# Kernel optimization log

Hardware: AMD Instinct MI355X
Metric: run time of the kernel (lower is better)

## Reference

```python
import jax, jax.numpy as jnp
import numpy as np

N = 50000          # nodes
E_RAW = 600000     # edges before self loops
FEAT = 64
HID = 64
HEADS = 4
NUM_SUBST = 32
NUM_GRAPHS = 128


def setup_inputs() -> dict:
    key = jax.random.key(0)
    ks = jax.random.split(key, 24)
    s = 0.05
    x = jax.random.normal(ks[0], (N, FEAT), jnp.float32)
    sids = jax.random.randint(ks[1], (N,), 0, NUM_SUBST)
    x = x.at[:, 5].set(sids.astype(jnp.float32))  # x[:,5] holds integer substructure ids
    edge_index = jax.random.randint(ks[2], (2, E_RAW), 0, N, dtype=jnp.int32)
    batch = jnp.sort(jax.random.randint(ks[3], (N,), 0, NUM_GRAPHS, dtype=jnp.int32))
    p = lambda i, shape: jax.random.normal(ks[i], shape, jnp.float32) * s
    return dict(
        x=x, edge_index=edge_index, batch=batch,
        # substructure attention MLP: Linear(FEAT,32) -> LeakyReLU(0.2) -> Linear(32,1)
        w_sa1=p(4, (FEAT, 32)), b_sa1=p(5, (32,)),
        w_sa2=p(6, (32, 1)), b_sa2=p(7, (1,)),
        # GATConv 1: in=FEAT+1, out=HID, heads=HEADS, concat
        W1=p(8, (FEAT + 1, HEADS * HID)), att_s1=p(9, (HEADS, HID)),
        att_d1=p(10, (HEADS, HID)), b1=p(11, (HEADS * HID,)),
        # GATConv 2: in=HEADS*HID, out=HID, heads=1
        W2=p(12, (HEADS * HID, HID)), att_s2=p(13, (1, HID)),
        att_d2=p(14, (1, HID)), b2=p(15, (HID,)),
        # prediction head
        Wp1=p(16, (HID, HID // 2)), bp1=p(17, (HID // 2,)),
        Wp2=p(18, (HID // 2, 1)), bp2=p(19, (1,)),
    )


def _gat_layer(h_in, src, dst, W, att_s, att_d, bias, n):
    heads, out_dim = att_s.shape
    h = (h_in @ W).reshape(n, heads, out_dim)            # [N, H, D]
    a_s = jnp.einsum('nhd,hd->nh', h, att_s)             # [N, H]
    a_d = jnp.einsum('nhd,hd->nh', h, att_d)
    e = jax.nn.leaky_relu(a_s[src] + a_d[dst], negative_slope=0.2)  # [E, H]
    m = jax.ops.segment_max(e, dst, num_segments=n)
    ex = jnp.exp(e - m[dst])
    denom = jax.ops.segment_sum(ex, dst, num_segments=n)
    alpha = ex / (denom[dst] + 1e-16)                    # segment softmax per dst node
    out = jax.ops.segment_sum(h[src] * alpha[..., None], dst, num_segments=n)
    return out.reshape(n, heads * out_dim) + bias        # concat heads + bias


def reference(x, edge_index, batch, w_sa1, b_sa1, w_sa2, b_sa2,
              W1, att_s1, att_d1, b1, W2, att_s2, att_d2, b2,
              Wp1, bp1, Wp2, bp2):
    n = x.shape[0]
    sid = jax.lax.stop_gradient(x[:, 5]).astype(jnp.int32)
    # segment mean of node features per substructure id (all NUM_SUBST ids present)
    cnt = jax.ops.segment_sum(jnp.ones((n,), x.dtype), sid, num_segments=NUM_SUBST)
    smean = jax.ops.segment_sum(x, sid, num_segments=NUM_SUBST) / jnp.maximum(cnt, 1.0)[:, None]
    logits = jax.nn.leaky_relu(smean @ w_sa1 + b_sa1, negative_slope=0.2) @ w_sa2 + b_sa2
    w = jax.nn.softmax(logits, axis=0)                   # [S, 1]
    atom_w = w[sid]                                      # broadcast back to atoms [N, 1]
    h = jnp.concatenate([x, atom_w], axis=1)             # [N, FEAT+1]
    # add_self_loops (gat2's remove+add self loops yields the same edge set)
    loops = jnp.arange(n, dtype=edge_index.dtype)
    src = jnp.concatenate([edge_index[0], loops])
    dst = jnp.concatenate([edge_index[1], loops])
    h = jax.nn.elu(_gat_layer(h, src, dst, W1, att_s1, att_d1, b1, n))
    h = _gat_layer(h, src, dst, W2, att_s2, att_d2, b2, n)
    g = jax.ops.segment_sum(h, batch, num_segments=NUM_GRAPHS)   # global_add_pool
    return jax.nn.elu(g @ Wp1 + bp1) @ Wp2 + bp2         # [NUM_GRAPHS, 1]
```

## Files before the change

### kernel.cpp

```cpp
#include <hip/hip_runtime.h>
#include <math.h>

#define N_NODES 50000
#define E_RAWN  600000
#define FEAT    64
#define HID     64
#define HEADS   4
#define NSUB    32
#define NGRAPH  128
#define NB_SCAN ((N_NODES + 255) / 256)
#define G2_NODES 128

__device__ __forceinline__ float leaky02(float v) { return v >= 0.f ? v : 0.2f * v; }
__device__ __forceinline__ float elu1(float v)    { return v > 0.f ? v : expm1f(v); }

__device__ __forceinline__ unsigned bf2pack(float a, float b) {
    unsigned ua = __float_as_uint(a), ub = __float_as_uint(b);
    ua = (ua + 0x7FFFu + ((ua >> 16) & 1u)) >> 16;
    ub = (ub + 0x7FFFu + ((ub >> 16) & 1u)) >> 16;
    return ua | (ub << 16);
}
__device__ __forceinline__ float bflo(unsigned p) { return __uint_as_float(p << 16); }
__device__ __forceinline__ float bfhi(unsigned p) { return __uint_as_float(p & 0xFFFF0000u); }
__device__ __forceinline__ float bfs(unsigned short v) { return __uint_as_float((unsigned)v << 16); }

__global__ void k_subst_accum(const float* __restrict__ x,
                              float* __restrict__ ssum, float* __restrict__ scnt) {
    __shared__ float lsum[NSUB * FEAT];
    __shared__ float lcnt[NSUB];
    int tid = threadIdx.x;
    for (int i = tid; i < NSUB * FEAT; i += blockDim.x) lsum[i] = 0.f;
    if (tid < NSUB) lcnt[tid] = 0.f;
    __syncthreads();
    const int total = N_NODES * FEAT;
    for (int idx = blockIdx.x * blockDim.x + tid; idx < total; idx += gridDim.x * blockDim.x) {
        int node = idx >> 6, f = idx & 63;
        int sid = (int)x[node * FEAT + 5];
        atomicAdd(&lsum[sid * FEAT + f], x[idx]);
        if (f == 0) atomicAdd(&lcnt[sid], 1.f);
    }
    __syncthreads();
    for (int i = tid; i < NSUB * FEAT; i += blockDim.x) atomicAdd(&ssum[i], lsum[i]);
    if (tid < NSUB) atomicAdd(&scnt[tid], lcnt[tid]);
}

__global__ void k_subst_mlp(const float* __restrict__ ssum, const float* __restrict__ scnt,
                            const float* __restrict__ w_sa1, const float* __restrict__ b_sa1,
                            const float* __restrict__ w_sa2, const float* __restrict__ b_sa2,
                            float* __restrict__ wsub) {
    __shared__ float logits[NSUB];
    int s = threadIdx.x;
    float cnt = fmaxf(scnt[s], 1.f);
    float sm[FEAT];
    for (int k = 0; k < FEAT; k++) sm[k] = ssum[s * FEAT + k] / cnt;
    float logit = b_sa2[0];
    for (int j = 0; j < 32; j++) {
        float hj = b_sa1[j];
        for (int k = 0; k < FEAT; k++) hj += sm[k] * w_sa1[k * 32 + j];
        hj = leaky02(hj);
        logit += hj * w_sa2[j];
    }
    logits[s] = logit;
    __syncthreads();
    float m = -1e30f;
    for (int i = 0; i < NSUB; i++) m = fmaxf(m, logits[i]);
    float dsum = 0.f;
    for (int i = 0; i < NSUB; i++) dsum += expf(logits[i] - m);
    wsub[s] = expf(logits[s] - m) / dsum;
}

__global__ __launch_bounds__(256) void k_gemm1(const float* __restrict__ x,
                                               const float* __restrict__ wsub,
                                               const float* __restrict__ W1,
                                               const float* __restrict__ att_s1,
                                               const float* __restrict__ att_d1,
                                               unsigned* __restrict__ h1b,
                                               float* __restrict__ as1, float* __restrict__ ad1) {
    __shared__ float xs[65][36];
    __shared__ float ws[16][260];
    int t = threadIdx.x;
    int gbase = blockIdx.x * 32;
    for (int idx = t; idx < 32 * 64; idx += 256) {
        int n = idx >> 6, f = idx & 63;
        int g = gbase + n;
        xs[f][n] = (g < N_NODES) ? x[(size_t)g * FEAT + f] : 0.f;
    }
    __syncthreads();
    if (t < 32) {
        int sid = (int)xs[5][t];
        xs[64][t] = wsub[sid & (NSUB - 1)];
    }

    int m = t & 31, q = t >> 5;
    int c0 = m * 8, n0 = q * 4;
    float accs[32];
    #pragma unroll
    for (int i = 0; i < 32; ++i) accs[i] = 0.f;

    for (int kc = 0; kc < 4; ++kc) {
        __syncthreads();
        #pragma unroll
        for (int s = 0; s < 16; ++s)
            ws[s][t] = W1[(size_t)(kc * 16 + s) * 256 + t];
        __syncthreads();
        #pragma unroll
        for (int kk = 0; kk < 16; ++kk) {
            float4 wa = *(const float4*)(&ws[kk][c0]);
            float4 wb = *(const float4*)(&ws[kk][c0 + 4]);
            float4 xv = *(const float4*)(&xs[kc * 16 + kk][n0]);
            float wv[8] = {wa.x, wa.y, wa.z, wa.w, wb.x, wb.y, wb.z, wb.w};
            float xj[4] = {xv.x, xv.y, xv.z, xv.w};
            #pragma unroll
            for (int c = 0; c < 8; ++c)
                #pragma unroll
                for (int j = 0; j < 4; ++j)
                    accs[c * 4 + j] += wv[c] * xj[j];
        }
    }
    {
        float4 wa = *(const float4*)(W1 + (size_t)64 * 256 + c0);
        float4 wb = *(const float4*)(W1 + (size_t)64 * 256 + c0 + 4);
        float4 xv = *(const float4*)(&xs[64][n0]);
        float wv[8] = {wa.x, wa.y, wa.z, wa.w, wb.x, wb.y, wb.z, wb.w};
        float xj[4] = {xv.x, xv.y, xv.z, xv.w};
        #pragma unroll
        for (int c = 0; c < 8; ++c)
            #pragma unroll
            for (int j = 0; j < 4; ++j)
                accs[c * 4 + j] += wv[c] * xj[j];
    }

    float atts[8], attd[8];
    #pragma unroll
    for (int c = 0; c < 8; ++c) { atts[c] = att_s1[c0 + c]; attd[c] = att_d1[c0 + c]; }
    int h = m >> 3;
    #pragma unroll
    for (int j = 0; j < 4; ++j) {
        int node = gbase + n0 + j;
        float ps = 0.f, pd = 0.f;
        #pragma unroll
        for (int c = 0; c < 8; ++c) { ps += accs[c * 4 + j] * atts[c]; pd += accs[c * 4 + j] * attd[c]; }
        ps += __shfl_xor(ps, 1, 64); pd += __shfl_xor(pd, 1, 64);
        ps += __shfl_xor(ps, 2, 64); pd += __shfl_xor(pd, 2, 64);
        ps += __shfl_xor(ps, 4, 64); pd += __shfl_xor(pd, 4, 64);
        if (node < N_NODES) {
            uint4 pk;
            pk.x = bf2pack(accs[0 * 4 + j], accs[1 * 4 + j]);
            pk.y = bf2pack(accs[2 * 4 + j], accs[3 * 4 + j]);
            pk.z = bf2pack(accs[4 * 4 + j], accs[5 * 4 + j]);
            pk.w = bf2pack(accs[6 * 4 + j], accs[7 * 4 + j]);
            *(uint4*)(h1b + (size_t)node * 128 + m * 4) = pk;
            if ((m & 7) == 0) { as1[node * 4 + h] = ps; ad1[node * 4 + h] = pd; }
        }
    }
}

__global__ void k_count(const int* __restrict__ dst, int* __restrict__ cnt) {
    int e = blockIdx.x * blockDim.x + threadIdx.x;
    if (e < E_RAWN) atomicAdd(&cnt[dst[e]], 1);
}

__global__ void k_scan1(const int* __restrict__ cnt, int* __restrict__ offs, int* __restrict__ bsum) {
    __shared__ int sd[256];
    int tid = threadIdx.x;
    int i = blockIdx.x * 256 + tid;
    int v = (i < N_NODES) ? cnt[i] : 0;
    sd[tid] = v;
    for (int off = 1; off < 256; off <<= 1) {
        __syncthreads();
        int tv = (tid >= off) ? sd[tid - off] : 0;
        __syncthreads();
        sd[tid] += tv;
    }
    __syncthreads();
    if (i < N_NODES) offs[i] = sd[tid] - v;
    if (tid == 255) bsum[blockIdx.x] = sd[255];
}

__global__ void k_scan2(int* __restrict__ bsum, int nb) {
    __shared__ int sd[256];
    int tid = threadIdx.x;
    int v = (tid < nb) ? bsum[tid] : 0;
    sd[tid] = v;
    for (int off = 1; off < 256; off <<= 1) {
        __syncthreads();
        int tv = (tid >= off) ? sd[tid - off] : 0;
        __syncthreads();
        sd[tid] += tv;
    }
    __syncthreads();
    if (tid < nb) bsum[tid] = sd[tid] - v;
}

__global__ void k_scan3(int* __restrict__ offs, const int* __restrict__ bsum) {
    int i = blockIdx.x * 256 + threadIdx.x;
    if (i < N_NODES) offs[i] += bsum[blockIdx.x];
    if (blockIdx.x == 0 && threadIdx.x == 0) offs[N_NODES] = E_RAWN;
}

__global__ void k_scatter(const int* __restrict__ src, const int* __restrict__ dst,
                          const int* __restrict__ offs, int* __restrict__ cur,
                          int* __restrict__ esrc) {
    int e = blockIdx.x * blockDim.x + threadIdx.x;
    if (e < E_RAWN) {
        int d = dst[e];
        int pos = offs[d] + atomicAdd(&cur[d], 1);
        esrc[pos] = src[e];
    }
}

__global__ __launch_bounds__(256) void k_gat1(const unsigned* __restrict__ h1b,
                                              const float* __restrict__ as1,
                                              const float* __restrict__ ad1,
                                              const int* __restrict__ offs,
                                              const int* __restrict__ esrc,
                                              const float* __restrict__ b1,
                                              unsigned* __restrict__ hactb) {
    int wave = threadIdx.x >> 6, lane = threadIdx.x & 63;
    int i = blockIdx.x * 4 + wave;
    if (i >= N_NODES) return;
    int beg = offs[i], end = offs[i + 1];
    int h = lane >> 4;
    float adv = ad1[i * 4 + h];
    float w0 = __expf(leaky02(as1[i * 4 + h] + adv));
    uint2 hv = *(const uint2*)(h1b + (size_t)i * 128 + lane * 2);
    float4 acc = make_float4(w0 * bflo(hv.x), w0 * bfhi(hv.x), w0 * bflo(hv.y), w0 * bfhi(hv.y));
    float d = w0;
    int p = beg;
    for (; p + 3 < end; p += 4) {
        int s0 = esrc[p], s1 = esrc[p + 1], s2 = esrc[p + 2], s3 = esrc[p + 3];
        uint2 hA = *(const uint2*)(h1b + (size_t)s0 * 128 + lane * 2);
        uint2 hB = *(const uint2*)(h1b + (size_t)s1 * 128 + lane * 2);
        uint2 hC = *(const uint2*)(h1b + (size_t)s2 * 128 + lane * 2);
        uint2 hD = *(const uint2*)(h1b + (size_t)s3 * 128 + lane * 2);
        float a0 = as1[s0 * 4 + h], a1 = as1[s1 * 4 + h];
        float a2 = as1[s2 * 4 + h], a3 = as1[s3 * 4 + h];
        float wA = __expf(leaky02(a0 + adv));
        float wB = __expf(leaky02(a1 + adv));
        float wC = __expf(leaky02(a2 + adv));
        float wD = __expf(leaky02(a3 + adv));
        d += (wA + wB) + (wC + wD);
        acc.x += wA * bflo(hA.x) + wB * bflo(hB.x) + wC * bflo(hC.x) + wD * bflo(hD.x);
        acc.y += wA * bfhi(hA.x) + wB * bfhi(hB.x) + wC * bfhi(hC.x) + wD * bfhi(hD.x);
        acc.z += wA * bflo(hA.y) + wB * bflo(hB.y) + wC * bflo(hC.y) + wD * bflo(hD.y);
        acc.w += wA * bfhi(hA.y) + wB * bfhi(hB.y) + wC * bfhi(hC.y) + wD * bfhi(hD.y);
    }
    for (; p < end; ++p) {
        int s0 = esrc[p];
        uint2 hA = *(const uint2*)(h1b + (size_t)s0 * 128 + lane * 2);
        float wA = __expf(leaky02(as1[s0 * 4 + h] + adv));
        d += wA;
        acc.x += wA * bflo(hA.x);
        acc.y += wA * bfhi(hA.x);
        acc.z += wA * bflo(hA.y);
        acc.w += wA * bfhi(hA.y);
    }
    float inv = 1.f / (d + 1e-16f);
    float4 bb = *(const float4*)(b1 + lane * 4);
    float rx = elu1(acc.x * inv + bb.x);
    float ry = elu1(acc.y * inv + bb.y);
    float rz = elu1(acc.z * inv + bb.z);
    float rw = elu1(acc.w * inv + bb.w);
    uint2 pk;
    pk.x = bf2pack(rx, ry);
    pk.y = bf2pack(rz, rw);
    *(uint2*)(hactb + (size_t)i * 128 + lane * 2) = pk;
}

__global__ __launch_bounds__(256) void k_gemm2(const unsigned* __restrict__ hactb,
                                               const float* __restrict__ W2,
                                               const float* __restrict__ att_s2,
                                               const float* __restrict__ att_d2,
                                               unsigned short* __restrict__ h2b,
                                               float* __restrict__ as2, float* __restrict__ ad2) {
    __shared__ float hs[G2_NODES][68];
    int t = threadIdx.x;
    int gbase = blockIdx.x * G2_NODES;
    int m = t & 7, q = t >> 3;
    int c0 = m * 8, n0 = q * 4;
    float accs[32];
    #pragma unroll
    for (int i = 0; i < 32; ++i) accs[i] = 0.f;

    int sn = t >> 3;
    int sko = t & 7;

    for (int kc = 0; kc < 4; ++kc) {
        __syncthreads();
        #pragma unroll
        for (int r = 0; r < 4; ++r) {
            int n = sn + r * 32;
            int g = gbase + n;
            uint4 v = (g < N_NODES)
                ? *(const uint4*)(hactb + (size_t)g * 128 + kc * 32 + sko * 4)
                : make_uint4(0u, 0u, 0u, 0u);
            float4 lo = make_float4(bflo(v.x), bfhi(v.x), bflo(v.y), bfhi(v.y));
            float4 hi = make_float4(bflo(v.z), bfhi(v.z), bflo(v.w), bfhi(v.w));
            *(float4*)(&hs[n][sko * 8])     = lo;
            *(float4*)(&hs[n][sko * 8 + 4]) = hi;
        }
        __syncthreads();
        const float* Wc = W2 + (size_t)kc * 64 * 64;
        for (int kk = 0; kk < 16; ++kk) {
            float4 xv0 = *(const float4*)(&hs[n0 + 0][kk * 4]);
            float4 xv1 = *(const float4*)(&hs[n0 + 1][kk * 4]);
            float4 xv2 = *(const float4*)(&hs[n0 + 2][kk * 4]);
            float4 xv3 = *(const float4*)(&hs[n0 + 3][kk * 4]);
            const float* x0 = (const float*)&xv0;
            const float* x1 = (const float*)&xv1;
            const float* x2 = (const float*)&xv2;
            const float* x3 = (const float*)&xv3;
            #pragma unroll
            for (int jj = 0; jj < 4; ++jj) {
                int k = kk * 4 + jj;
                float4 wa = *(const float4*)(Wc + (size_t)k * 64 + c0);
                float4 wb = *(const float4*)(Wc + (size_t)k * 64 + c0 + 4);
                float wv[8] = {wa.x, wa.y, wa.z, wa.w, wb.x, wb.y, wb.z, wb.w};
                float xj[4] = {x0[jj], x1[jj], x2[jj], x3[jj]};
                #pragma unroll
                for (int c = 0; c < 8; ++c)
                    #pragma unroll
                    for (int j = 0; j < 4; ++j)
                        accs[c * 4 + j] += wv[c] * xj[j];
            }
        }
    }

    float atts[8], attd[8];
    #pragma unroll
    for (int c = 0; c < 8; ++c) { atts[c] = att_s2[c0 + c]; attd[c] = att_d2[c0 + c]; }
    #pragma unroll
    for (int j = 0; j < 4; ++j) {
        int node = gbase + n0 + j;
        float ps = 0.f, pd = 0.f;
        #pragma unroll
        for (int c = 0; c < 8; ++c) { ps += accs[c * 4 + j] * atts[c]; pd += accs[c * 4 + j] * attd[c]; }
        ps += __shfl_xor(ps, 1, 64); pd += __shfl_xor(pd, 1, 64);
        ps += __shfl_xor(ps, 2, 64); pd += __shfl_xor(pd, 2, 64);
        ps += __shfl_xor(ps, 4, 64); pd += __shfl_xor(pd, 4, 64);
        if (node < N_NODES) {
            uint4 pk;
            pk.x = bf2pack(accs[0 * 4 + j], accs[1 * 4 + j]);
            pk.y = bf2pack(accs[2 * 4 + j], accs[3 * 4 + j]);
            pk.z = bf2pack(accs[4 * 4 + j], accs[5 * 4 + j]);
            pk.w = bf2pack(accs[6 * 4 + j], accs[7 * 4 + j]);
            *(uint4*)(h2b + (size_t)node * 64 + c0) = pk;
            if (m == 0) { as2[node] = ps; ad2[node] = pd; }
        }
    }
}

__global__ __launch_bounds__(256) void k_gat2(const unsigned short* __restrict__ h2b,
                                              const float* __restrict__ as2,
                                              const float* __restrict__ ad2,
                                              const int* __restrict__ offs,
                                              const int* __restrict__ esrc,
                                              float* __restrict__ rbuf) {
    int wave = threadIdx.x >> 6, lane = threadIdx.x & 63;
    int i = blockIdx.x * 4 + wave;
    if (i >= N_NODES) return;
    int beg = offs[i], end = offs[i + 1];
    float adv = ad2[i];
    float w0 = __expf(leaky02(as2[i] + adv));
    float d = w0;
    float acc = w0 * bfs(h2b[(size_t)i * 64 + lane]);
    int p = beg;
    for (; p + 3 < end; p += 4) {
        int s0 = esrc[p], s1 = esrc[p + 1], s2 = esrc[p + 2], s3 = esrc[p + 3];
        float hA = bfs(h2b[(size_t)s0 * 64 + lane]);
        float hB = bfs(h2b[(size_t)s1 * 64 + lane]);
        float hC = bfs(h2b[(size_t)s2 * 64 + lane]);
        float hD = bfs(h2b[(size_t)s3 * 64 + lane]);
        float wA = __expf(leaky02(as2[s0] + adv));
        float wB = __expf(leaky02(as2[s1] + adv));
        float wC = __expf(leaky02(as2[s2] + adv));
        float wD = __expf(leaky02(as2[s3] + adv));
        d += (wA + wB) + (wC + wD);
        acc += wA * hA + wB * hB + wC * hC + wD * hD;
    }
    for (; p < end; ++p) {
        int s0 = esrc[p];
        float wA = __expf(leaky02(as2[s0] + adv));
        d += wA;
        acc += wA * bfs(h2b[(size_t)s0 * 64 + lane]);
    }
    rbuf[(size_t)i * 64 + lane] = acc / (d + 1e-16f);
}

__device__ __forceinline__ int lower_bound_i(const int* a, int n, int v) {
    int lo = 0, hi = n;
    while (lo < hi) { int mid = (lo + hi) >> 1; if (a[mid] < v) lo = mid + 1; else hi = mid; }
    return lo;
}

__global__ void k_pool_head(const float* __restrict__ rbuf, const int* __restrict__ batch,
                            const float* __restrict__ b2,
                            const float* __restrict__ Wp1, const float* __restrict__ bp1,
                            const float* __restrict__ Wp2, const float* __restrict__ bp2,
                            float* __restrict__ out) {
    __shared__ float red[4][64];
    __shared__ float tot[64];
    __shared__ float hred[32];
    int b = blockIdx.x;
    int lo = lower_bound_i(batch, N_NODES, b);
    int hi = lower_bound_i(batch, N_NODES, b + 1);
    int t = threadIdx.x;
    int c = t & 63, rg = t >> 6;
    float s = 0.f;
    for (int r = lo + rg; r < hi; r += 4) s += rbuf[(size_t)r * 64 + c];
    red[rg][c] = s;
    __syncthreads();
    if (rg == 0) tot[c] = red[0][c] + red[1][c] + red[2][c] + red[3][c] + (float)(hi - lo) * b2[c];
    __syncthreads();
    if (t < 32) {
        float hj = bp1[t];
        #pragma unroll
        for (int k = 0; k < 64; ++k) hj += tot[k] * Wp1[k * 32 + t];
        hred[t] = elu1(hj) * Wp2[t];
    }
    __syncthreads();
    if (t == 0) {
        float a = bp2[0];
        #pragma unroll
        for (int j = 0; j < 32; ++j) a += hred[j];
        out[b] = a;
    }
}

extern "C" void kernel_launch(void* const* d_in, const int* in_sizes, int n_in,
                              void* d_out, int out_size, void* d_ws, size_t ws_size,
                              hipStream_t stream) {
    const float* x      = (const float*)d_in[0];
    const int*   edge   = (const int*)d_in[1];
    const int*   batch  = (const int*)d_in[2];
    const float* w_sa1  = (const float*)d_in[3];
    const float* b_sa1  = (const float*)d_in[4];
    const float* w_sa2  = (const float*)d_in[5];
    const float* b_sa2  = (const float*)d_in[6];
    const float* W1     = (const float*)d_in[7];
    const float* att_s1 = (const float*)d_in[8];
    const float* att_d1 = (const float*)d_in[9];
    const float* b1     = (const float*)d_in[10];
    const float* W2     = (const float*)d_in[11];
    const float* att_s2 = (const float*)d_in[12];
    const float* att_d2 = (const float*)d_in[13];
    const float* b2     = (const float*)d_in[14];
    const float* Wp1    = (const float*)d_in[15];
    const float* bp1    = (const float*)d_in[16];
    const float* Wp2    = (const float*)d_in[17];
    const float* bp2    = (const float*)d_in[18];
    float* out = (float*)d_out;

    const int* e_src = edge;
    const int* e_dst = edge + E_RAWN;

    char* base = (char*)d_ws;
    size_t off = 0;
    auto alloc = [&](size_t bytes) -> void* {
        void* p = base + off;
        off = (off + bytes + 255) & ~(size_t)255;
        return p;
    };
    float* ssum   = (float*)alloc((NSUB * FEAT + NSUB) * 4);
    float* scnt   = ssum + NSUB * FEAT;
    float* wsub   = (float*)alloc(NSUB * 4);
    float* as1    = (float*)alloc((size_t)N_NODES * 4 * 4);
    float* ad1    = (float*)alloc((size_t)N_NODES * 4 * 4);
    float* as2    = (float*)alloc((size_t)N_NODES * 4);
    float* ad2    = (float*)alloc((size_t)N_NODES * 4);
    int*   counts = (int*)alloc((size_t)N_NODES * 2 * 4);
    int*   cursor = counts + N_NODES;
    int*   offs   = (int*)alloc((size_t)(N_NODES + 1) * 4);
    int*   bsum   = (int*)alloc(256 * 4);
    int*   esrc   = (int*)alloc((size_t)E_RAWN * 4);
    unsigned* h1b   = (unsigned*)alloc((size_t)N_NODES * 128 * 4);
    unsigned* hactb = (unsigned*)alloc((size_t)N_NODES * 128 * 4);
    unsigned short* h2b = (unsigned short*)alloc((size_t)N_NODES * 64 * 2);
    float* rbuf   = (float*)alloc((size_t)N_NODES * 64 * 4);

    (void)hipMemsetAsync(ssum,   0, (NSUB * FEAT + NSUB) * 4, stream);
    (void)hipMemsetAsync(counts, 0, (size_t)N_NODES * 2 * 4, stream);

    k_subst_accum<<<256, 256, 0, stream>>>(x, ssum, scnt);
    k_subst_mlp<<<1, 32, 0, stream>>>(ssum, scnt, w_sa1, b_sa1, w_sa2, b_sa2, wsub);
    k_gemm1<<<(N_NODES + 31) / 32, 256, 0, stream>>>(x, wsub, W1, att_s1, att_d1, h1b, as1, ad1);

    k_count<<<(E_RAWN + 255) / 256, 256, 0, stream>>>(e_dst, counts);
    k_scan1<<<NB_SCAN, 256, 0, stream>>>(counts, offs, bsum);
    k_scan2<<<1, 256, 0, stream>>>(bsum, NB_SCAN);
    k_scan3<<<NB_SCAN, 256, 0, stream>>>(offs, bsum);
    k_scatter<<<(E_RAWN + 255) / 256, 256, 0, stream>>>(e_src, e_dst, offs, cursor, esrc);

    k_gat1<<<(N_NODES + 3) / 4, 256, 0, stream>>>(h1b, as1, ad1, offs, esrc, b1, hactb);
    k_gemm2<<<(N_NODES + G2_NODES - 1) / G2_NODES, 256, 0, stream>>>(hactb, W2, att_s2, att_d2, h2b, as2, ad2);
    k_gat2<<<(N_NODES + 3) / 4, 256, 0, stream>>>(h2b, as2, ad2, offs, esrc, rbuf);
    k_pool_head<<<NGRAPH, 256, 0, stream>>>(rbuf, batch, b2, Wp1, bp1, Wp2, bp2, out);
}
```

Measured before the change: 309.0 us.

## Fuse prep kernels and enlarge gemm1 node tile to 64

Merges the substructure accumulation with the destination-degree count into one launch by splitting blocks by role, and merges the substructure MLP with the first scan stage the same way. This removes two kernel launches and lets independent work run concurrently. Separately, gemm1 now processes 64 nodes per block with 64 accumulators per thread, which halves the number of W1 tile loads but raises register pressure and may lower occupancy.

Result: faster. 298.4 us (-3.4%).

```diff
diff --git a/kernel.cpp b/kernel.cpp
--- a/kernel.cpp
+++ b/kernel.cpp
@@ -24,49 +24,77 @@
 __device__ __forceinline__ float bfhi(unsigned p) { return __uint_as_float(p & 0xFFFF0000u); }
 __device__ __forceinline__ float bfs(unsigned short v) { return __uint_as_float((unsigned)v << 16); }
 
-__global__ void k_subst_accum(const float* __restrict__ x,
-                              float* __restrict__ ssum, float* __restrict__ scnt) {
-    __shared__ float lsum[NSUB * FEAT];
-    __shared__ float lcnt[NSUB];
+__global__ void k_prep(const float* __restrict__ x,
+                       float* __restrict__ ssum, float* __restrict__ scnt,
+                       const int* __restrict__ dst, int* __restrict__ cnt) {
     int tid = threadIdx.x;
-    for (int i = tid; i < NSUB * FEAT; i += blockDim.x) lsum[i] = 0.f;
-    if (tid < NSUB) lcnt[tid] = 0.f;
-    __syncthreads();
-    const int total = N_NODES * FEAT;
-    for (int idx = blockIdx.x * blockDim.x + tid; idx < total; idx += gridDim.x * blockDim.x) {
-        int node = idx >> 6, f = idx & 63;
-        int sid = (int)x[node * FEAT + 5];
-        atomicAdd(&lsum[sid * FEAT + f], x[idx]);
-        if (f == 0) atomicAdd(&lcnt[sid], 1.f);
-    }
-    __syncthreads();
-    for (int i = tid; i < NSUB * FEAT; i += blockDim.x) atomicAdd(&ssum[i], lsum[i]);
-    if (tid < NSUB) atomicAdd(&scnt[tid], lcnt[tid]);
-}
-
-__global__ void k_subst_mlp(const float* __restrict__ ssum, const float* __restrict__ scnt,
+    if (blockIdx.x < 256) {
+        __shared__ float lsum[NSUB * FEAT];
+        __shared__ float lcnt[NSUB];
+        for (int i = tid; i < NSUB * FEAT; i += 256) lsum[i] = 0.f;
+        if (tid < NSUB) lcnt[tid] = 0.f;
+        __syncthreads();
+        const int total = N_NODES * FEAT;
+        for (int idx = blockIdx.x * 256 + tid; idx < total; idx += 256 * 256) {
+            int node = idx >> 6, f = idx & 63;
+            int sid = (int)x[node * FEAT + 5];
+            atomicAdd(&lsum[sid * FEAT + f], x[idx]);
+            if (f == 0) atomicAdd(&lcnt[sid], 1.f);
+        }
+        __syncthreads();
+        for (int i = tid; i < NSUB * FEAT; i += 256) atomicAdd(&ssum[i], lsum[i]);
+        if (tid < NSUB) atomicAdd(&scnt[tid], lcnt[tid]);
+    } else {
+        for (int e = (blockIdx.x - 256) * 256 + tid; e < E_RAWN; e += 256 * 256)
+            atomicAdd(&cnt[dst[e]], 1);
+    }
+}
+
+__global__ void k_mlp_scan1(const int* __restrict__ cnt, int* __restrict__ offs, int* __restrict__ bsum,
+                            const float* __restrict__ ssum, const float* __restrict__ scnt,
                             const float* __restrict__ w_sa1, const float* __restrict__ b_sa1,
                             const float* __restrict__ w_sa2, const float* __restrict__ b_sa2,
                             float* __restrict__ wsub) {
-    __shared__ float logits[NSUB];
-    int s = threadIdx.x;
-    float cnt = fmaxf(scnt[s], 1.f);
-    float sm[FEAT];
-    for (int k = 0; k < FEAT; k++) sm[k] = ssum[s * FEAT + k] / cnt;
-    float logit = b_sa2[0];
-    for (int j = 0; j < 32; j++) {
-        float hj = b_sa1[j];
-        for (int k = 0; k < FEAT; k++) hj += sm[k] * w_sa1[k * 32 + j];
-        hj = leaky02(hj);
-        logit += hj * w_sa2[j];
-    }
-    logits[s] = logit;
+    int tid = threadIdx.x;
+    if (blockIdx.x == NB_SCAN) {
+        __shared__ float logits[NSUB];
+        int s = tid;
+        if (s < NSUB) {
+            float c = fmaxf(scnt[s], 1.f);
+            float sm[FEAT];
+            for (int k = 0; k < FEAT; k++) sm[k] = ssum[s * FEAT + k] / c;
+            float logit = b_sa2[0];
+            for (int j = 0; j < 32; j++) {
+                float hj = b_sa1[j];
+                for (int k = 0; k < FEAT; k++) hj += sm[k] * w_sa1[k * 32 + j];
+                hj = leaky02(hj);
+                logit += hj * w_sa2[j];
+            }
+            logits[s] = logit;
+        }
+        __syncthreads();
+        if (s < NSUB) {
+            float m = -1e30f;
+            for (int i = 0; i < NSUB; i++) m = fmaxf(m, logits[i]);
+            float dsum = 0.f;
+            for (int i = 0; i < NSUB; i++) dsum += expf(logits[i] - m);
+            wsub[s] = expf(logits[s] - m) / dsum;
+        }
+        return;
+    }
+    __shared__ int sd[256];
+    int i = blockIdx.x * 256 + tid;
+    int v = (i < N_NODES) ? cnt[i] : 0;
+    sd[tid] = v;
+    for (int off = 1; off < 256; off <<= 1) {
+        __syncthreads();
+        int tv = (tid >= off) ? sd[tid - off] : 0;
+        __syncthreads();
+        sd[tid] += tv;
+    }
     __syncthreads();
-    float m = -1e30f;
-    for (int i = 0; i < NSUB; i++) m = fmaxf(m, logits[i]);
-    float dsum = 0.f;
-    for (int i = 0; i < NSUB; i++) dsum += expf(logits[i] - m);
-    wsub[s] = expf(logits[s] - m) / dsum;
+    if (i < N_NODES) offs[i] = sd[tid] - v;
+    if (tid == 255) bsum[blockIdx.x] = sd[255];
 }
 
 __global__ __launch_bounds__(256) void k_gemm1(const float* __restrict__ x,
@@ -76,26 +104,26 @@
                                                const float* __restrict__ att_d1,
                                                unsigned* __restrict__ h1b,
                                                float* __restrict__ as1, float* __restrict__ ad1) {
-    __shared__ float xs[65][36];
+    __shared__ float xs[65][68];
     __shared__ float ws[16][260];
     int t = threadIdx.x;
-    int gbase = blockIdx.x * 32;
-    for (int idx = t; idx < 32 * 64; idx += 256) {
+    int gbase = blockIdx.x * 64;
+    for (int idx = t; idx < 64 * 64; idx += 256) {
         int n = idx >> 6, f = idx & 63;
         int g = gbase + n;
         xs[f][n] = (g < N_NODES) ? x[(size_t)g * FEAT + f] : 0.f;
     }
     __syncthreads();
-    if (t < 32) {
+    if (t < 64) {
         int sid = (int)xs[5][t];
         xs[64][t] = wsub[sid & (NSUB - 1)];
     }
 
     int m = t & 31, q = t >> 5;
-    int c0 = m * 8, n0 = q * 4;
-    float accs[32];
+    int c0 = m * 8, q8 = q * 8;
+    float accs[64];
     #pragma unroll
-    for (int i = 0; i < 32; ++i) accs[i] = 0.f;
+    for (int i = 0; i < 64; ++i) accs[i] = 0.f;
 
     for (int kc = 0; kc < 4; ++kc) {
         __syncthreads();
@@ -107,27 +135,29 @@
         for (int kk = 0; kk < 16; ++kk) {
             float4 wa = *(const float4*)(&ws[kk][c0]);
             float4 wb = *(const float4*)(&ws[kk][c0 + 4]);
-            float4 xv = *(const float4*)(&xs[kc * 16 + kk][n0]);
+            float4 xa = *(const float4*)(&xs[kc * 16 + kk][q8]);
+            float4 xb = *(const float4*)(&xs[kc * 16 + kk][q8 + 4]);
             float wv[8] = {wa.x, wa.y, wa.z, wa.w, wb.x, wb.y, wb.z, wb.w};
-            float xj[4] = {xv.x, xv.y, xv.z, xv.w};
+            float xv[8] = {xa.x, xa.y, xa.z, xa.w, xb.x, xb.y, xb.z, xb.w};
             #pragma unroll
             for (int c = 0; c < 8; ++c)
                 #pragma unroll
-                for (int j = 0; j < 4; ++j)
-                    accs[c * 4 + j] += wv[c] * xj[j];
+                for (int j = 0; j < 8; ++j)
+                    accs[c * 8 + j] += wv[c] * xv[j];
         }
     }
     {
         float4 wa = *(const float4*)(W1 + (size_t)64 * 256 + c0);
         float4 wb = *(const float4*)(W1 + (size_t)64 * 256 + c0 + 4);
-        float4 xv = *(const float4*)(&xs[64][n0]);
+        float4 xa = *(const float4*)(&xs[64][q8]);
+        float4 xb = *(const float4*)(&xs[64][q8 + 4]);
         float wv[8] = {wa.x, wa.y, wa.z, wa.w, wb.x, wb.y, wb.z, wb.w};
-        float xj[4] = {xv.x, xv.y, xv.z, xv.w};
+        float xv[8] = {xa.x, xa.y, xa.z, xa.w, xb.x, xb.y, xb.z, xb.w};
         #pragma unroll
         for (int c = 0; c < 8; ++c)
             #pragma unroll
-            for (int j = 0; j < 4; ++j)
-                accs[c * 4 + j] += wv[c] * xj[j];
+            for (int j = 0; j < 8; ++j)
+                accs[c * 8 + j] += wv[c] * xv[j];
     }
 
     float atts[8], attd[8];
@@ -135,46 +165,24 @@
     for (int c = 0; c < 8; ++c) { atts[c] = att_s1[c0 + c]; attd[c] = att_d1[c0 + c]; }
     int h = m >> 3;
     #pragma unroll
-    for (int j = 0; j < 4; ++j) {
-        int node = gbase + n0 + j;
+    for (int j = 0; j < 8; ++j) {
+        int node = gbase + q8 + j;
         float ps = 0.f, pd = 0.f;
         #pragma unroll
-        for (int c = 0; c < 8; ++c) { ps += accs[c * 4 + j] * atts[c]; pd += accs[c * 4 + j] * attd[c]; }
+        for (int c = 0; c < 8; ++c) { ps += accs[c * 8 + j] * atts[c]; pd += accs[c * 8 + j] * attd[c]; }
         ps += __shfl_xor(ps, 1, 64); pd += __shfl_xor(pd, 1, 64);
         ps += __shfl_xor(ps, 2, 64); pd += __shfl_xor(pd, 2, 64);
         ps += __shfl_xor(ps, 4, 64); pd += __shfl_xor(pd, 4, 64);
         if (node < N_NODES) {
             uint4 pk;
-            pk.x = bf2pack(accs[0 * 4 + j], accs[1 * 4 + j]);
-            pk.y = bf2pack(accs[2 * 4 + j], accs[3 * 4 + j]);
-            pk.z = bf2pack(accs[4 * 4 + j], accs[5 * 4 + j]);
-            pk.w = bf2pack(accs[6 * 4 + j], accs[7 * 4 + j]);
+            pk.x = bf2pack(accs[0 * 8 + j], accs[1 * 8 + j]);
+            pk.y = bf2pack(accs[2 * 8 + j], accs[3 * 8 + j]);
+            pk.z = bf2pack(accs[4 * 8 + j], accs[5 * 8 + j]);
+            pk.w = bf2pack(accs[6 * 8 + j], accs[7 * 8 + j]);
             *(uint4*)(h1b + (size_t)node * 128 + m * 4) = pk;
             if ((m & 7) == 0) { as1[node * 4 + h] = ps; ad1[node * 4 + h] = pd; }
         }
     }
-}
-
-__global__ void k_count(const int* __restrict__ dst, int* __restrict__ cnt) {
-    int e = blockIdx.x * blockDim.x + threadIdx.x;
-    if (e < E_RAWN) atomicAdd(&cnt[dst[e]], 1);
-}
-
-__global__ void k_scan1(const int* __restrict__ cnt, int* __restrict__ offs, int* __restrict__ bsum) {
-    __shared__ int sd[256];
-    int tid = threadIdx.x;
-    int i = blockIdx.x * 256 + tid;
-    int v = (i < N_NODES) ? cnt[i] : 0;
-    sd[tid] = v;
-    for (int off = 1; off < 256; off <<= 1) {
-        __syncthreads();
-        int tv = (tid >= off) ? sd[tid - off] : 0;
-        __syncthreads();
-        sd[tid] += tv;
-    }
-    __syncthreads();
-    if (i < N_NODES) offs[i] = sd[tid] - v;
-    if (tid == 255) bsum[blockIdx.x] = sd[255];
 }
 
 __global__ void k_scan2(int* __restrict__ bsum, int nb) {
@@ -481,12 +489,11 @@
     (void)hipMemsetAsync(ssum,   0, (NSUB * FEAT + NSUB) * 4, stream);
     (void)hipMemsetAsync(counts, 0, (size_t)N_NODES * 2 * 4, stream);
 
-    k_subst_accum<<<256, 256, 0, stream>>>(x, ssum, scnt);
-    k_subst_mlp<<<1, 32, 0, stream>>>(ssum, scnt, w_sa1, b_sa1, w_sa2, b_sa2, wsub);
-    k_gemm1<<<(N_NODES + 31) / 32, 256, 0, stream>>>(x, wsub, W1, att_s1, att_d1, h1b, as1, ad1);
-
-    k_count<<<(E_RAWN + 255) / 256, 256, 0, stream>>>(e_dst, counts);
-    k_scan1<<<NB_SCAN, 256, 0, stream>>>(counts, offs, bsum);
+    k_prep<<<512, 256, 0, stream>>>(x, ssum, scnt, e_dst, counts);
+    k_mlp_scan1<<<NB_SCAN + 1, 256, 0, stream>>>(counts, offs, bsum,
+                                                 ssum, scnt, w_sa1, b_sa1, w_sa2, b_sa2, wsub);
+    k_gemm1<<<(N_NODES + 63) / 64, 256, 0, stream>>>(x, wsub, W1, att_s1, att_d1, h1b, as1, ad1);
+
     k_scan2<<<1, 256, 0, stream>>>(bsum, NB_SCAN);
     k_scan3<<<NB_SCAN, 256, 0, stream>>>(offs, bsum);
     k_scatter<<<(E_RAWN + 255) / 256, 256, 0, stream>>>(e_src, e_dst, offs, cursor, esrc);
```
